# Kernel tuning notes

Hardware: AMD Instinct MI355X
Metric: run time of the kernel (lower is better)

## Reference

```python
import jax, jax.numpy as jnp
import numpy as np

NUM_HEADS = 16
FIELD_SIZE = 512
SIGMA = 3.0
EMB = 1024


def _causal_kernel_fft(G, sigma):
    # kernel[i] = exp(-|i - G//2| / sigma) for i < G//2, else 0; normalized
    i = np.arange(G)
    dist = np.abs(i - G // 2)
    kernel = np.where(i >= G // 2, 0.0, np.exp(-dist / sigma)).astype(np.float32)
    kernel = kernel / (kernel.sum() + 1e-8)
    return jnp.asarray(np.fft.rfft(kernel), dtype=jnp.complex64)


def setup_inputs() -> dict:
    key = jax.random.key(0)
    ks = jax.random.split(key, 9)
    B, N, D = 4, 4096, EMB
    s = 1.0 / np.sqrt(D)
    return {
        "x": jax.random.normal(ks[0], (B, N, D), dtype=jnp.float32),
        "q_w": jax.random.uniform(ks[1], (D, D), minval=-s, maxval=s, dtype=jnp.float32),
        "q_b": jnp.zeros((D,), jnp.float32),
        "k_w": jax.random.uniform(ks[2], (D, D), minval=-s, maxval=s, dtype=jnp.float32),
        "k_b": jnp.zeros((D,), jnp.float32),
        "v_w": jax.random.uniform(ks[3], (D, D), minval=-s, maxval=s, dtype=jnp.float32),
        "v_b": jnp.zeros((D,), jnp.float32),
        "out_w": jax.random.uniform(ks[4], (D, D), minval=-s, maxval=s, dtype=jnp.float32),
        "out_b": jnp.zeros((D,), jnp.float32),
    }


def reference(x, q_w, q_b, k_w, k_b, v_w, v_b, out_w, out_b):
    B, N, D = x.shape
    H, hd, G = NUM_HEADS, D // NUM_HEADS, FIELD_SIZE

    # projections (q is computed in the original but unused downstream)
    q = x @ q_w.T + q_b  # noqa: F841 (faithful to original)
    k = (x @ k_w.T + k_b).reshape(B, N, H, hd).transpose(0, 2, 1, 3)  # (B,H,N,hd)
    v = (x @ v_w.T + v_b).reshape(B, N, H, hd).transpose(0, 2, 1, 3)

    # map sequence positions -> field bins (same for all b, h)
    pos = jnp.arange(N, dtype=jnp.float32) / max(N - 1, 1) * (G - 1)
    field_idx = jnp.clip(pos.astype(jnp.int32), 0, G - 1)  # (N,)

    # weighted values by key magnitude
    k_mag = jnp.linalg.norm(k, axis=-1, keepdims=True)  # (B,H,N,1)
    wv = v * k_mag  # (B,H,N,hd)

    # scatter-add tokens into field bins (vectorized over B,H,hd)
    field = jax.ops.segment_sum(wv.transpose(2, 0, 1, 3), field_idx,
                                num_segments=G)  # (G,B,H,hd)
    field = field.transpose(1, 2, 0, 3)  # (B,H,G,hd)

    # causal convolution along the field via FFT (circular, as in original)
    kfft = _causal_kernel_fft(G, SIGMA)
    f_fft = jnp.fft.rfft(field, n=G, axis=2)
    conv = jnp.fft.irfft(f_fft * kfft[None, None, :, None], n=G, axis=2)

    # gather back to token positions
    out = conv[:, :, field_idx, :]  # (B,H,N,hd)
    out = out.transpose(0, 2, 1, 3).reshape(B, N, D)
    return out @ out_w.T + out_b
```

## Files before the change

kernel.cpp:

```cpp
#include <hip/hip_runtime.h>
#include <hip/hip_bf16.h>

#define NPOS 4096
#define DIM  1024
#define GSZ  512

#define GAS __attribute__((address_space(1)))
#define LAS __attribute__((address_space(3)))

typedef __attribute__((ext_vector_type(8))) short bf16x8;
typedef __attribute__((ext_vector_type(4))) float f32x4;

__device__ __forceinline__ void async_load16(const void* g, void* l) {
  __builtin_amdgcn_global_load_lds((const GAS void*)g, (LAS void*)l, 16, 0, 0);
}

__device__ __forceinline__ int fidx_of(int n) {
  return (int)(((float)n / 4095.0f) * 511.0f);
}

__device__ __forceinline__ float bf2f(unsigned short s) {
  union { unsigned u; float f; } v; v.u = ((unsigned)s) << 16; return v.f;
}

__device__ __forceinline__ void bin_range(int g, int& i0, int& i1) {
  i0 = (g * 4095 + 510) / 511;
  while (i0 > 0 && fidx_of(i0 - 1) >= g) --i0;
  while (i0 < NPOS && fidx_of(i0) < g) ++i0;
  if (g == GSZ - 1) { i1 = NPOS; return; }
  i1 = ((g + 1) * 4095 + 510) / 511;
  while (i1 > 0 && fidx_of(i1 - 1) >= g + 1) --i1;
  while (i1 < NPOS && fidx_of(i1) < g + 1) ++i1;
}

__global__ __launch_bounds__(256) void cast_all(
    const float* __restrict__ x, const float* __restrict__ kw,
    const float* __restrict__ vw, const float* __restrict__ ow,
    __hip_bfloat16* __restrict__ xb, __hip_bfloat16* __restrict__ kvwb,
    __hip_bfloat16* __restrict__ outwb) {
  int blk = blockIdx.x;
  const float* src; __hip_bfloat16* dst; int off;
  if (blk < 16384)      { src = x;  dst = xb;              off = blk; }
  else if (blk < 17408) { src = kw; dst = kvwb;            off = blk - 16384; }
  else if (blk < 18432) { src = vw; dst = kvwb + 1048576;  off = blk - 17408; }
  else                  { src = ow; dst = outwb;           off = blk - 18432; }
  int i = (off * 256 + threadIdx.x) * 4;
  float4 f = *(const float4*)(src + i);
  ushort4 o;
  __hip_bfloat16 t;
  t = __float2bfloat16(f.x); o.x = *(unsigned short*)&t;
  t = __float2bfloat16(f.y); o.y = *(unsigned short*)&t;
  t = __float2bfloat16(f.z); o.z = *(unsigned short*)&t;
  t = __float2bfloat16(f.w); o.w = *(unsigned short*)&t;
  *(ushort4*)(dst + i) = o;
}


#define BAR()   __builtin_amdgcn_s_barrier()
#define LGKM0() do { asm volatile("s_waitcnt lgkmcnt(0)" ::: "memory"); \
                     __builtin_amdgcn_sched_barrier(0); } while (0)
#define VMW(N)  asm volatile("s_waitcnt vmcnt(" #N ")" ::: "memory")

#define STAGE(BUF, KT) do { \
    const __hip_bfloat16* ag_ = ag0 + (KT) * 64; \
    const __hip_bfloat16* bg_ = bg0 + (KT) * 64; \
    _Pragma("unroll") \
    for (int c_ = 0; c_ < 4; ++c_) { \
      async_load16(ag_ + (size_t)c_ * 65536, &As[BUF][c_ * 4096 + ldst]); \
      async_load16(bg_ + (size_t)c_ * 65536, &Bs[BUF][c_ * 4096 + ldst]); \
    } \
  } while (0)

#define LDA(BUF, MT, CB) (*(const bf16x8*)&As[BUF][abase + (MT) * 1024 + (CB)])
#define LDB(BUF, NT, CB) (*(const bf16x8*)&Bs[BUF][bbase + (NT) * 1024 + (CB)])

#define MFMA_Q(MQ, NQ, BF) do { \
    __builtin_amdgcn_s_setprio(1); \
    _Pragma("unroll") \
    for (int m_ = 0; m_ < 4; ++m_) { \
      _Pragma("unroll") \
      for (int n_ = 0; n_ < 2; ++n_) { \
        acc[(MQ)*4+m_][(NQ)*2+n_] = __builtin_amdgcn_mfma_f32_16x16x32_bf16( \
            af[m_][0], BF[n_][0], acc[(MQ)*4+m_][(NQ)*2+n_], 0, 0, 0); \
        acc[(MQ)*4+m_][(NQ)*2+n_] = __builtin_amdgcn_mfma_f32_16x16x32_bf16( \
            af[m_][1], BF[n_][1], acc[(MQ)*4+m_][(NQ)*2+n_], 0, 0, 0); \
      } \
    } \
    __builtin_amdgcn_s_setprio(0); \
  } while (0)

#define DO_TILE(BUF, KT) do { \
     \
    _Pragma("unroll") \
    for (int m_ = 0; m_ < 4; ++m_) { af[m_][0] = LDA(BUF, m_, cb0); af[m_][1] = LDA(BUF, m_, cb1); } \
    _Pragma("unroll") \
    for (int n_ = 0; n_ < 2; ++n_) { b0f[n_][0] = LDB(BUF, n_, cb0); b0f[n_][1] = LDB(BUF, n_, cb1); } \
    BAR(); LGKM0(); \
    MFMA_Q(0, 0, b0f); \
    BAR(); \
     \
    _Pragma("unroll") \
    for (int n_ = 0; n_ < 2; ++n_) { b1f[n_][0] = LDB(BUF, 2 + n_, cb0); b1f[n_][1] = LDB(BUF, 2 + n_, cb1); } \
    BAR(); LGKM0(); \
    MFMA_Q(0, 1, b1f); \
    BAR(); \
     \
    _Pragma("unroll") \
    for (int m_ = 0; m_ < 4; ++m_) { af[m_][0] = LDA(BUF, 4 + m_, cb0); af[m_][1] = LDA(BUF, 4 + m_, cb1); } \
    BAR(); LGKM0(); \
    MFMA_Q(1, 1, b1f); \
    BAR(); \
     \
    if ((KT) + 2 < 16) STAGE(BUF, (KT) + 2); \
    BAR(); \
    MFMA_Q(1, 0, b0f); \
    if ((KT) + 2 < 16) { VMW(8); } else if ((KT) == 14) { VMW(0); } \
    BAR(); \
  } while (0)

__global__ __launch_bounds__(512, 2) void gemm_kv(
    const __hip_bfloat16* __restrict__ A,
    const __hip_bfloat16* __restrict__ B,
    const float* __restrict__ k_b, const float* __restrict__ v_b,
    __hip_bfloat16* __restrict__ Vb, float* __restrict__ knorm) {
  __shared__ __align__(16) __hip_bfloat16 As[2][16384];
  __shared__ __align__(16) __hip_bfloat16 Bs[2][16384];
  const int tid = threadIdx.x;

  const int l  = blockIdx.y * 64 + blockIdx.x;
  const int vv = (l & 7) * 64 + (l >> 3);
  const int bx = vv & 63, by = vv >> 6;
  const int bm = bx * 256;

  const int sb  = ((((tid & 7) * 16) ^ (((tid >> 3) & 7) << 4)) >> 1);
  const int r0  = tid >> 3;
  const __hip_bfloat16* ag0 = A + (size_t)(bm + r0) * 1024 + sb;
  const __hip_bfloat16* bg0 = B + (size_t)(by * 256 + r0) * 1024 + sb;
  const int ldst = tid * 8;

  const int wave = tid >> 6, lane = tid & 63;
  const int wr = wave >> 2, wc = wave & 3;
  const int m16 = lane & 15, quad = lane >> 4;
  const int swz  = (m16 & 7) << 4;
  const int cb0  = ((quad * 16)      ^ swz) >> 1;
  const int cb1  = ((quad * 16 + 64) ^ swz) >> 1;
  const int abase = wr * 8192 + m16 * 64;
  const int bbase = wc * 4096 + m16 * 64;

  f32x4 acc[8][4];
#pragma unroll
  for (int i = 0; i < 8; i++)
#pragma unroll
    for (int j = 0; j < 4; j++) acc[i][j] = (f32x4)0.f;

  bf16x8 af[4][2], b0f[2][2], b1f[2][2];

  STAGE(0, 0);
  STAGE(1, 1);
  VMW(8);
  BAR();

  for (int kt = 0; kt < 16; kt += 2) {
    DO_TILE(0, kt);
    DO_TILE(1, kt + 1);
  }

  if (by < 4) {
    const int head = by * 4 + wc;
    float bv[4];
#pragma unroll
    for (int nt = 0; nt < 4; nt++) bv[nt] = k_b[by * 256 + wc * 64 + nt * 16 + m16];
#pragma unroll
    for (int mt = 0; mt < 8; mt++) {
#pragma unroll
      for (int r = 0; r < 4; r++) {
        float s = 0.f;
#pragma unroll
        for (int nt = 0; nt < 4; nt++) {
          float t = acc[mt][nt][r] + bv[nt];
          s += t * t;
        }
        s += __shfl_xor(s, 1);
        s += __shfl_xor(s, 2);
        s += __shfl_xor(s, 4);
        s += __shfl_xor(s, 8);
        if (m16 == 0) {
          int row = bm + wr * 128 + mt * 16 + quad * 4 + r;
          knorm[(size_t)row * 16 + head] = sqrtf(s);
        }
      }
    }
  } else {
    const int colb = (by - 4) * 256 + wc * 64;
#pragma unroll
    for (int mt = 0; mt < 8; mt++) {
#pragma unroll
      for (int nt = 0; nt < 4; nt++) {
        int col = colb + nt * 16 + m16;
        float bvv = v_b[col];
#pragma unroll
        for (int r = 0; r < 4; r++) {
          int row = bm + wr * 128 + mt * 16 + quad * 4 + r;
          Vb[(size_t)row * 1024 + col] = __float2bfloat16(acc[mt][nt][r] + bvv);
        }
      }
    }
  }
}

__global__ __launch_bounds__(256) void gemm_outc(
    const __hip_bfloat16* __restrict__ A,
    const __hip_bfloat16* __restrict__ B,
    const float* __restrict__ bias,
    float* __restrict__ C) {
  const int K = 1024;
  __shared__ __align__(16) __hip_bfloat16 Aso[64 * 32];
  __shared__ __align__(16) __hip_bfloat16 Bso[64 * 32];
  const int tid = threadIdx.x;
  const int bm = blockIdx.x * 64, bn = blockIdx.y * 64;

  const int srow = tid >> 2;
  const int scol = (tid & 3) * 8;
  const __hip_bfloat16* ap = A + (size_t)(bm + srow) * K + scol;
  const __hip_bfloat16* bp = B + (size_t)(bn + srow) * K + scol;
  __hip_bfloat16* as = &Aso[srow * 32 + scol];
  __hip_bfloat16* bs = &Bso[srow * 32 + scol];

  const int wave = tid >> 6, lane = tid & 63;
  const int wm = (wave >> 1) * 32, wn = (wave & 1) * 32;
  const int m16 = lane & 15, quad = lane >> 4;

  f32x4 acc[2][2];
#pragma unroll
  for (int i = 0; i < 2; i++)
#pragma unroll
    for (int j = 0; j < 2; j++) acc[i][j] = (f32x4)0.f;

  for (int k0 = 0; k0 < K; k0 += 32) {
    async_load16(ap + k0, as);
    async_load16(bp + k0, bs);
    __syncthreads();
    bf16x8 afr[2], bfr[2];
#pragma unroll
    for (int mt = 0; mt < 2; mt++)
      afr[mt] = *(const bf16x8*)&Aso[(wm + mt * 16 + m16) * 32 + quad * 8];
#pragma unroll
    for (int nt = 0; nt < 2; nt++)
      bfr[nt] = *(const bf16x8*)&Bso[(wn + nt * 16 + m16) * 32 + quad * 8];
#pragma unroll
    for (int mt = 0; mt < 2; mt++)
#pragma unroll
      for (int nt = 0; nt < 2; nt++)
        acc[mt][nt] = __builtin_amdgcn_mfma_f32_16x16x32_bf16(afr[mt], bfr[nt], acc[mt][nt], 0, 0, 0);
    __syncthreads();
  }

#pragma unroll
  for (int mt = 0; mt < 2; mt++) {
#pragma unroll
    for (int nt = 0; nt < 2; nt++) {
      int col = bn + wn + nt * 16 + m16;
      float bv = bias[col];
#pragma unroll
      for (int r = 0; r < 4; r++) {
        int row = bm + wm + mt * 16 + quad * 4 + r;
        C[(size_t)row * 1024 + col] = acc[mt][nt][r] + bv;
      }
    }
  }
}

__global__ __launch_bounds__(256) void gather_out_kernel(
    const float* __restrict__ outc, float* __restrict__ out) {
  const int row = blockIdx.x;
  const int b = row >> 12, n = row & (NPOS - 1);
  const int g = fidx_of(n);
  const float4* src = (const float4*)(outc + ((size_t)(b * GSZ) + g) * DIM);
  float4* dst = (float4*)(out + (size_t)row * DIM);
  dst[threadIdx.x] = src[threadIdx.x];
}

__global__ __launch_bounds__(256) void wv_field_kernel(
    const __hip_bfloat16* __restrict__ V, const float* __restrict__ knorm,
    float* __restrict__ field) {
  const int b = blockIdx.x, g = blockIdx.y;
  int i0, i1;
  bin_range(g, i0, i1);
  int cnt = i1 - i0;
  if (cnt > 9) cnt = 9;
  __shared__ float km[9][16];
  const int tid = threadIdx.x;
  if (tid < 144) {
    int r = tid >> 4, h = tid & 15;
    km[r][h] = (r < cnt) ? knorm[(size_t)(b * NPOS + i0 + r) * 16 + h] : 0.f;
  }
  __syncthreads();
  const int c0 = tid * 4, h = tid >> 4;
  const unsigned short* vbase = (const unsigned short*)V + (size_t)(b * NPOS + i0) * 1024 + c0;
  ushort4 vv[8];
  float ww[8];
#pragma unroll
  for (int j = 0; j < 8; ++j) {
    int jc = (j < cnt) ? j : 0;
    vv[j] = *(const ushort4*)(vbase + (size_t)jc * 1024);
    ww[j] = (j < cnt) ? km[j][h] : 0.f;
  }
  float a0 = 0.f, a1 = 0.f, a2 = 0.f, a3 = 0.f;
#pragma unroll
  for (int j = 0; j < 8; ++j) {
    a0 += ww[j] * bf2f(vv[j].x); a1 += ww[j] * bf2f(vv[j].y);
    a2 += ww[j] * bf2f(vv[j].z); a3 += ww[j] * bf2f(vv[j].w);
  }
  if (cnt == 9) {
    ushort4 v8 = *(const ushort4*)(vbase + (size_t)8 * 1024);
    float w8 = km[8][h];
    a0 += w8 * bf2f(v8.x); a1 += w8 * bf2f(v8.y);
    a2 += w8 * bf2f(v8.z); a3 += w8 * bf2f(v8.w);
  }
  *(float4*)(field + ((size_t)(b * GSZ + g)) * DIM + c0) = make_float4(a0, a1, a2, a3);
}

__global__ __launch_bounds__(256) void conv_ema_kernel(
    const float* __restrict__ field, __hip_bfloat16* __restrict__ convb) {
  const int b = blockIdx.x, h = blockIdx.y, n0 = blockIdx.z * 64;
  __shared__ float slab[128 * 64];
  const int tid = threadIdx.x;
  const float* fb = field + (size_t)b * GSZ * DIM + h * 64;
  for (int i = tid; i < 128 * 16; i += 256) {
    int row = i >> 4, c4 = i & 15;
    int gg = (n0 + 257 + row) & (GSZ - 1);
    *(float4*)&slab[row * 64 + c4 * 4] = *(const float4*)(fb + (size_t)gg * DIM + c4 * 4);
  }
  __syncthreads();
  const float a = 0.71653131057378927f;
  const float w1 = 1.0f - a;
  const int c = tid & 63, sub = tid >> 6;
  const int e0 = sub * 16;
  float acc = 0.f;
#pragma unroll 4
  for (int t = e0 + 79; t >= e0 + 16; --t)
    acc = w1 * slab[t * 64 + c] + a * acc;
#pragma unroll
  for (int t = e0 + 15; t >= e0; --t) {
    acc = w1 * slab[t * 64 + c] + a * acc;
    convb[((size_t)(b * GSZ) + n0 + t) * DIM + h * 64 + c] = __float2bfloat16(acc);
  }
}

extern "C" void kernel_launch(void* const* d_in, const int* in_sizes, int n_in,
                              void* d_out, int out_size, void* d_ws, size_t ws_size,
                              hipStream_t stream) {
  (void)in_sizes; (void)n_in; (void)out_size; (void)ws_size;
  const float* x     = (const float*)d_in[0];
  const float* k_w   = (const float*)d_in[3];
  const float* k_b   = (const float*)d_in[4];
  const float* v_w   = (const float*)d_in[5];
  const float* v_b   = (const float*)d_in[6];
  const float* out_w = (const float*)d_in[7];
  const float* out_b = (const float*)d_in[8];

  char* p = (char*)d_ws;
  __hip_bfloat16* xb    = (__hip_bfloat16*)p;
  float*          outc  = (float*)p;          p += (size_t)16384 * 1024 * 2;
  __hip_bfloat16* kvwb  = (__hip_bfloat16*)p; p += (size_t)2048 * 1024 * 2;
  __hip_bfloat16* outwb = (__hip_bfloat16*)p; p += (size_t)1024 * 1024 * 2;
  __hip_bfloat16* Vb    = (__hip_bfloat16*)p; p += (size_t)16384 * 1024 * 2;
  float*          knorm = (float*)p;          p += (size_t)16384 * 16 * 4;
  float*          field = (float*)p;          p += (size_t)4 * 512 * 1024 * 4;
  __hip_bfloat16* convb = (__hip_bfloat16*)p;

  cast_all<<<19456, 256, 0, stream>>>(x, k_w, v_w, out_w, xb, kvwb, outwb);

  gemm_kv<<<dim3(64, 8), 512, 0, stream>>>(xb, kvwb, k_b, v_b, Vb, knorm);

  wv_field_kernel<<<dim3(4, 512), 256, 0, stream>>>(Vb, knorm, field);
  conv_ema_kernel<<<dim3(4, 16, 8), 256, 0, stream>>>(field, convb);

  gemm_outc<<<dim3(32, 16), 256, 0, stream>>>(convb, outwb, out_b, outc);
  gather_out_kernel<<<16384, 256, 0, stream>>>(outc, (float*)d_out);
}
```

Baseline: 264.1 us.

## Fuse gather into output GEMM epilogue and interleave KV GEMM prefetch loads

```diff
diff --git a/kernel.cpp b/kernel.cpp
--- a/kernel.cpp
+++ b/kernel.cpp
@@ -61,13 +61,16 @@
                      __builtin_amdgcn_sched_barrier(0); } while (0)
 #define VMW(N)  asm volatile("s_waitcnt vmcnt(" #N ")" ::: "memory")
 
-#define STAGE(BUF, KT) do { \
-    const __hip_bfloat16* ag_ = ag0 + (KT) * 64; \
-    const __hip_bfloat16* bg_ = bg0 + (KT) * 64; \
+#define STAGE_A(BUF, KT, C) \
+  async_load16(ag0 + (size_t)(KT) * 64 + (size_t)(C) * 65536, &As[BUF][(C) * 4096 + ldst])
+#define STAGE_B(BUF, KT, C) \
+  async_load16(bg0 + (size_t)(KT) * 64 + (size_t)(C) * 65536, &Bs[BUF][(C) * 4096 + ldst])
+
+#define STAGE_FULL(BUF, KT) do { \
     _Pragma("unroll") \
     for (int c_ = 0; c_ < 4; ++c_) { \
-      async_load16(ag_ + (size_t)c_ * 65536, &As[BUF][c_ * 4096 + ldst]); \
-      async_load16(bg_ + (size_t)c_ * 65536, &Bs[BUF][c_ * 4096 + ldst]); \
+      STAGE_A(BUF, KT, c_); \
+      STAGE_B(BUF, KT, c_); \
     } \
   } while (0)
 
@@ -90,6 +93,7 @@
   } while (0)
 
 #define DO_TILE(BUF, KT) do { \
+    const bool pf_ = (KT) + 2 < 16; \
      \
     _Pragma("unroll") \
     for (int m_ = 0; m_ < 4; ++m_) { af[m_][0] = LDA(BUF, m_, cb0); af[m_][1] = LDA(BUF, m_, cb1); } \
@@ -101,20 +105,22 @@
      \
     _Pragma("unroll") \
     for (int n_ = 0; n_ < 2; ++n_) { b1f[n_][0] = LDB(BUF, 2 + n_, cb0); b1f[n_][1] = LDB(BUF, 2 + n_, cb1); } \
+    if (pf_) { STAGE_A(BUF, (KT) + 2, 0); STAGE_A(BUF, (KT) + 2, 2); } \
     BAR(); LGKM0(); \
     MFMA_Q(0, 1, b1f); \
     BAR(); \
      \
     _Pragma("unroll") \
     for (int m_ = 0; m_ < 4; ++m_) { af[m_][0] = LDA(BUF, 4 + m_, cb0); af[m_][1] = LDA(BUF, 4 + m_, cb1); } \
+    if (pf_) { STAGE_B(BUF, (KT) + 2, 0); STAGE_B(BUF, (KT) + 2, 1); \
+               STAGE_B(BUF, (KT) + 2, 2); STAGE_B(BUF, (KT) + 2, 3); } \
     BAR(); LGKM0(); \
     MFMA_Q(1, 1, b1f); \
     BAR(); \
      \
-    if ((KT) + 2 < 16) STAGE(BUF, (KT) + 2); \
-    BAR(); \
+    if (pf_) { STAGE_A(BUF, (KT) + 2, 1); STAGE_A(BUF, (KT) + 2, 3); } \
     MFMA_Q(1, 0, b0f); \
-    if ((KT) + 2 < 16) { VMW(8); } else if ((KT) == 14) { VMW(0); } \
+    if (pf_) { VMW(8); } else if ((KT) == 14) { VMW(0); } \
     BAR(); \
   } while (0)
 
@@ -155,8 +161,8 @@
 
   bf16x8 af[4][2], b0f[2][2], b1f[2][2];
 
-  STAGE(0, 0);
-  STAGE(1, 1);
+  STAGE_FULL(0, 0);
+  STAGE_FULL(1, 1);
   VMW(8);
   BAR();
 
@@ -258,26 +264,21 @@
 #pragma unroll
   for (int mt = 0; mt < 2; mt++) {
 #pragma unroll
-    for (int nt = 0; nt < 2; nt++) {
-      int col = bn + wn + nt * 16 + m16;
-      float bv = bias[col];
-#pragma unroll
-      for (int r = 0; r < 4; r++) {
-        int row = bm + wm + mt * 16 + quad * 4 + r;
-        C[(size_t)row * 1024 + col] = acc[mt][nt][r] + bv;
+    for (int r = 0; r < 4; r++) {
+      int row = bm + wm + mt * 16 + quad * 4 + r;
+      int bb = row >> 9, g = row & (GSZ - 1);
+      int i0, i1;
+      bin_range(g, i0, i1);
+      float* obase = C + ((size_t)bb << 12) * DIM;
+#pragma unroll
+      for (int nt = 0; nt < 2; nt++) {
+        int col = bn + wn + nt * 16 + m16;
+        float val = acc[mt][nt][r] + bias[col];
+        for (int n = i0; n < i1; ++n)
+          obase[(size_t)n * DIM + col] = val;
       }
     }
   }
-}
-
-__global__ __launch_bounds__(256) void gather_out_kernel(
-    const float* __restrict__ outc, float* __restrict__ out) {
-  const int row = blockIdx.x;
-  const int b = row >> 12, n = row & (NPOS - 1);
-  const int g = fidx_of(n);
-  const float4* src = (const float4*)(outc + ((size_t)(b * GSZ) + g) * DIM);
-  float4* dst = (float4*)(out + (size_t)row * DIM);
-  dst[threadIdx.x] = src[threadIdx.x];
 }
 
 __global__ __launch_bounds__(256) void wv_field_kernel(
@@ -360,8 +361,7 @@
   const float* out_b = (const float*)d_in[8];
 
   char* p = (char*)d_ws;
-  __hip_bfloat16* xb    = (__hip_bfloat16*)p;
-  float*          outc  = (float*)p;          p += (size_t)16384 * 1024 * 2;
+  __hip_bfloat16* xb    = (__hip_bfloat16*)p;         p += (size_t)16384 * 1024 * 2;
   __hip_bfloat16* kvwb  = (__hip_bfloat16*)p; p += (size_t)2048 * 1024 * 2;
   __hip_bfloat16* outwb = (__hip_bfloat16*)p; p += (size_t)1024 * 1024 * 2;
   __hip_bfloat16* Vb    = (__hip_bfloat16*)p; p += (size_t)16384 * 1024 * 2;
@@ -376,6 +376,5 @@
   wv_field_kernel<<<dim3(4, 512), 256, 0, stream>>>(Vb, knorm, field);
   conv_ema_kernel<<<dim3(4, 16, 8), 256, 0, stream>>>(field, convb);
 
-  gemm_outc<<<dim3(32, 16), 256, 0, stream>>>(convb, outwb, out_b, outc);
-  gather_out_kernel<<<16384, 256, 0, stream>>>(outc, (float*)d_out);
-}
+  gemm_outc<<<dim3(32, 16), 256, 0, stream>>>(convb, outwb, out_b, (float*)d_out);
+}
```

Result: no change. 261.5 us (-1.0%).
